# Optimization experiments

Measured on AMD Instinct MI355X. Metric: run time of the kernel, lower is better.

Reference implementation:

```python
import jax, jax.numpy as jnp
import numpy as np

N_HEAD = 16
D_MODEL = 2048
ROPE_BASE = 10000.0


def setup_inputs() -> dict:
    key = jax.random.key(0)
    k1, k2, k3 = jax.random.split(key, 3)
    b, s, d = 2, 2048, D_MODEL
    x = jax.random.normal(k1, (b, s, d), dtype=jnp.float32)
    # torch nn.Linear init scale ~ 1/sqrt(fan_in); keep activations sane
    W_qkv = jax.random.normal(k2, (3 * d, d), dtype=jnp.float32) * (d ** -0.5)
    W_o = jax.random.normal(k3, (d, d), dtype=jnp.float32) * (d ** -0.5)
    return {"x": x, "W_qkv": W_qkv, "W_o": W_o}


def _rotate_half(x):
    x1, x2 = jnp.split(x, 2, axis=-1)
    return jnp.concatenate((-x2, x1), axis=-1)


def _rope_cos_sin(seq_len, d_head, dtype):
    inv_freq = 1.0 / (ROPE_BASE ** (jnp.arange(0, d_head, 2, dtype=jnp.float32) / d_head))
    t = jnp.arange(seq_len, dtype=jnp.float32)
    freqs = jnp.einsum("i,j->ij", t, inv_freq)          # [s, d_head/2]
    emb = jnp.concatenate((freqs, freqs), axis=-1)       # [s, d_head]
    return jnp.cos(emb).astype(dtype)[None, None], jnp.sin(emb).astype(dtype)[None, None]


def reference(x, W_qkv, W_o):
    b, s, d = x.shape
    h = N_HEAD
    dh = d // h
    qkv = x @ W_qkv.T                                    # [b, s, 3d]
    qkv = qkv.reshape(b, s, 3, h, dh)
    q, k, v = (jnp.transpose(qkv[:, :, i], (0, 2, 1, 3)) for i in range(3))  # [b, h, s, dh]
    cos, sin = _rope_cos_sin(s, dh, x.dtype)
    q = q * cos + _rotate_half(q) * sin
    k = k * cos + _rotate_half(k) * sin
    scale = dh ** -0.5
    scores = jnp.einsum("bhqd,bhkd->bhqk", q, k) * scale  # [b, h, s, s]
    causal = jnp.tril(jnp.ones((s, s), dtype=bool))
    scores = jnp.where(causal[None, None], scores, jnp.finfo(scores.dtype).min)
    attn = jax.nn.softmax(scores, axis=-1)
    z = jnp.einsum("bhqk,bhkd->bhqd", attn, v)            # [b, h, s, dh]
    z = jnp.transpose(z, (0, 2, 1, 3)).reshape(b, s, d)
    return z @ W_o.T
```

## Files before the change

### kernel.cpp

```cpp
#include <hip/hip_runtime.h>
#include <stdint.h>
#include <stddef.h>

typedef __attribute__((ext_vector_type(8))) short bf16x8;
typedef __attribute__((ext_vector_type(4))) float f32x4;
typedef __attribute__((ext_vector_type(16))) float f32x16;
typedef __attribute__((ext_vector_type(4))) unsigned int u32x4;

#define AS1 __attribute__((address_space(1)))
#define AS3 __attribute__((address_space(3)))

__device__ __forceinline__ void gll16(const void* g, void* l) {
  __builtin_amdgcn_global_load_lds((const AS1 unsigned int*)g, (AS3 unsigned int*)l, 16, 0, 0);
}

__device__ __forceinline__ uint16_t f2bf(float f) {
  uint32_t u = __builtin_bit_cast(uint32_t, f);
  u += 0x7fffu + ((u >> 16) & 1u);
  return (uint16_t)(u >> 16);
}
__device__ __forceinline__ float bf2f(uint16_t h) {
  uint32_t u = ((uint32_t)h) << 16;
  return __builtin_bit_cast(float, u);
}
__device__ __forceinline__ uint32_t pack2bf(float lo, float hi) {
  return (uint32_t)f2bf(lo) | ((uint32_t)f2bf(hi) << 16);
}

#define BARRIER() do { asm volatile("" ::: "memory"); __builtin_amdgcn_s_barrier(); asm volatile("" ::: "memory"); } while (0)

__global__ void cvt_all(const float* __restrict__ x, const float* __restrict__ wqkv,
                        const float* __restrict__ wo,
                        uint16_t* __restrict__ xb, uint16_t* __restrict__ wqkvb,
                        uint16_t* __restrict__ wob) {
  int i = blockIdx.x * blockDim.x + threadIdx.x;
  const float* in; uint16_t* out; int off;
  if (i < 1048576)      { in = x;    out = xb;    off = i; }
  else if (i < 2621440) { in = wqkv; out = wqkvb; off = i - 1048576; }
  else                  { in = wo;   out = wob;   off = i - 2621440; }
  float4 a = reinterpret_cast<const float4*>(in)[2 * off];
  float4 b = reinterpret_cast<const float4*>(in)[2 * off + 1];
  union { uint16_t h[8]; u32x4 v; } u;
  u.h[0] = f2bf(a.x); u.h[1] = f2bf(a.y); u.h[2] = f2bf(a.z); u.h[3] = f2bf(a.w);
  u.h[4] = f2bf(b.x); u.h[5] = f2bf(b.y); u.h[6] = f2bf(b.z); u.h[7] = f2bf(b.w);
  reinterpret_cast<u32x4*>(out)[off] = u.v;
}

__global__ void rope_table(float* __restrict__ cosT, float* __restrict__ sinT) {
  int idx = blockIdx.x * blockDim.x + threadIdx.x;
  int s = idx >> 6, i = idx & 63;
  float invf = expf(-(float)i * (9.2103403719761836f / 64.0f));
  float f = (float)s * invf;
  cosT[idx] = cosf(f);
  sinT[idx] = sinf(f);
}

__global__ void rope_apply2(uint16_t* __restrict__ Qb, uint16_t* __restrict__ Kb,
                            const float* __restrict__ cosT, const float* __restrict__ sinT) {
  int idx = blockIdx.x * blockDim.x + threadIdx.x;
  uint16_t* buf = (idx < 4194304) ? Qb : Kb;
  int id = idx & 4194303;
  int i = id & 63;
  int s = (id >> 6) & 2047;
  int bh = id >> 17;
  size_t base = ((size_t)bh * 2048 + s) * 128;
  float x0 = bf2f(buf[base + i]);
  float x1 = bf2f(buf[base + i + 64]);
  float c = cosT[(s << 6) + i], sn = sinT[(s << 6) + i];
  buf[base + i]      = f2bf(x0 * c - x1 * sn);
  buf[base + i + 64] = f2bf(x1 * c + x0 * sn);
}

__global__ __launch_bounds__(512, 2) void gemm_qkv(
    const uint16_t* __restrict__ A,
    const uint16_t* __restrict__ B,
    uint16_t* __restrict__ Qb, uint16_t* __restrict__ Kb, uint16_t* __restrict__ Vt) {
  extern __shared__ uint16_t L[];
  const int t = threadIdx.x, lane = t & 63, w = t >> 6;
  const int fr = lane & 15, fg = lane >> 4;
  const int wm = w >> 2, wn = w & 3;
  const int flat = blockIdx.y * 16 + blockIdx.x;
  const int swz = (flat & 7) * 64 + (flat >> 3);
  const int m0 = (swz & 15) * 256, n0 = (swz >> 4) * 192;

  f32x4 acc[8][3];
#pragma unroll
  for (int i = 0; i < 8; i++)
#pragma unroll
    for (int j = 0; j < 3; j++) acc[i][j] = (f32x4)(0.0f);

#define STA(kt, half)                                                             \
  do {                                                                            \
    if ((kt) < 32) {                                                              \
      int g0_ = m0 + (half) * 128;                                                \
      uint16_t* dst_ = &L[((kt) & 1) * 28672 + (half) * 8192];                    \
      _Pragma("unroll")                                                           \
      for (int j_ = 0; j_ < 2; ++j_) {                                            \
        int c_ = t + j_ * 512;                                                    \
        int row_ = c_ >> 3, cc_ = c_ & 7, scc_ = cc_ ^ (row_ & 7);                \
        gll16(&A[(size_t)(g0_ + row_) * 2048 + (kt) * 64 + scc_ * 8],             \
              &dst_[(c_ & ~63) * 8]);                                             \
      }                                                                           \
    }                                                                             \
  } while (0)

#define STB(kt)                                                                   \
  do {                                                                            \
    if ((kt) < 32) {                                                              \
      uint16_t* dst_ = &L[((kt) & 1) * 28672 + 16384];                            \
      _Pragma("unroll")                                                           \
      for (int j_ = 0; j_ < 3; ++j_) {                                            \
        int c_ = t + j_ * 512;                                                    \
        int row_ = c_ >> 3, cc_ = c_ & 7, scc_ = cc_ ^ (row_ & 7);                \
        gll16(&B[(size_t)(n0 + row_) * 2048 + (kt) * 64 + scc_ * 8],              \
              &dst_[(c_ & ~63) * 8]);                                             \
      }                                                                           \
    }                                                                             \
  } while (0)

  auto LDA4 = [&](bf16x8 (&af)[8], int buf, int mh) {
#pragma unroll
    for (int mi = 0; mi < 4; ++mi)
#pragma unroll
      for (int ks = 0; ks < 2; ++ks) {
        int lr = (mh * 4 + mi) * 16 + fr;
        int ck = (ks * 4 + fg) ^ (lr & 7);
        af[mi * 2 + ks] = *(const bf16x8*)&L[buf * 28672 + wm * 8192 + lr * 64 + ck * 8];
      }
  };
  auto LDB = [&](bf16x8* bfr, int buf, int ni0, int nn) {
#pragma unroll
    for (int ni = 0; ni < 2; ++ni) {
      if (ni >= nn) break;
#pragma unroll
      for (int ks = 0; ks < 2; ++ks) {
        int rn = wn * 48 + (ni0 + ni) * 16 + fr;
        int ck = (ks * 4 + fg) ^ (rn & 7);
        bfr[ni * 2 + ks] = *(const bf16x8*)&L[buf * 28672 + 16384 + rn * 64 + ck * 8];
      }
    }
  };
  auto MF = [&](bf16x8 (&af)[8], bf16x8* bfr, int mh, int ni0, int nn) {
    __builtin_amdgcn_s_setprio(1);
#pragma unroll
    for (int mi = 0; mi < 4; ++mi)
#pragma unroll
      for (int ni = 0; ni < 2; ++ni) {
        if (ni >= nn) break;
#pragma unroll
        for (int ks = 0; ks < 2; ++ks)
          acc[mh * 4 + mi][ni0 + ni] = __builtin_amdgcn_mfma_f32_16x16x32_bf16(
              af[mi * 2 + ks], bfr[ni * 2 + ks], acc[mh * 4 + mi][ni0 + ni], 0, 0, 0);
      }
    __builtin_amdgcn_s_setprio(0);
  };

  STA(0, 0); STA(0, 1); STB(0); STA(1, 0);
  asm volatile("s_waitcnt vmcnt(2)" ::: "memory");
  BARRIER();

  for (int tl = 0; tl < 32; ++tl) {
    const int buf = tl & 1;
    bf16x8 af[8], bA[4], bB[4];
    LDA4(af, buf, 0); LDB(bA, buf, 0, 2); STA(tl + 1, 1);
    BARRIER(); MF(af, bA, 0, 0, 2); BARRIER();
    LDB(bB, buf, 2, 1); STB(tl + 1);
    BARRIER(); MF(af, bB, 0, 2, 1); BARRIER();
    LDA4(af, buf, 1);
    BARRIER(); MF(af, bA, 1, 0, 2); BARRIER();
    STA(tl + 2, 0);
    BARRIER(); MF(af, bB, 1, 2, 1);
    if (tl < 30) asm volatile("s_waitcnt vmcnt(2)" ::: "memory");
    else         asm volatile("s_waitcnt vmcnt(0)" ::: "memory");
    BARRIER();
  }
#undef STA
#undef STB

#pragma unroll
  for (int mi = 0; mi < 8; ++mi) {
#pragma unroll
    for (int ni = 0; ni < 3; ++ni) {
      int ng = n0 + wn * 48 + ni * 16 + fr;
      int head = (ng >> 7) & 15, dd = ng & 127;
      if (ng < 4096) {
        uint16_t* dst = (ng < 2048) ? Qb : Kb;
#pragma unroll
        for (int r = 0; r < 4; r++) {
          int mg = m0 + wm * 128 + mi * 16 + fg * 4 + r;
          int b = mg >> 11, si = mg & 2047;
          dst[((size_t)(b * 16 + head) * 2048 + si) * 128 + dd] = f2bf(acc[mi][ni][r]);
        }
      } else {
        uint2 pv = make_uint2(pack2bf(acc[mi][ni][0], acc[mi][ni][1]),
                              pack2bf(acc[mi][ni][2], acc[mi][ni][3]));
        int mg = m0 + wm * 128 + mi * 16 + fg * 4;
        int b = mg >> 11, si = mg & 2047;
        *(uint2*)&Vt[((size_t)(b * 16 + head) * 128 + dd) * 2048 + si] = pv;
      }
    }
  }
}

__global__ __launch_bounds__(256) void gemm_out_k(
    const uint16_t* __restrict__ A,
    const uint16_t* __restrict__ B,
    float* __restrict__ C) {
  __shared__ uint16_t Ash[3][128 * 32];
  __shared__ uint16_t Bsh[3][128 * 32];
  const int t = threadIdx.x;
  const int lane = t & 63;
  const int w = t >> 6, wr = w >> 1, wc = w & 1;
  const int fr = lane & 15, fg = lane >> 4, fk = fg * 8;
  const int m0 = blockIdx.x * 128, n0 = blockIdx.y * 128;
  const int K = 2048;
  const int T = K / 32;
  const int c0 = t, c1 = t + 256;

  f32x4 acc[4][4];
#pragma unroll
  for (int i = 0; i < 4; i++)
#pragma unroll
    for (int j = 0; j < 4; j++) acc[i][j] = (f32x4)(0.0f);

#define OUT_STAGE(tile, buf)                                                        \
  {                                                                                 \
    int kt_ = (tile) * 32;                                                          \
    gll16(&A[(size_t)(m0 + (c0 >> 2)) * K + kt_ + (c0 & 3) * 8], &Ash[buf][(c0 & ~63) * 8]); \
    gll16(&A[(size_t)(m0 + (c1 >> 2)) * K + kt_ + (c1 & 3) * 8], &Ash[buf][(c1 & ~63) * 8]); \
    gll16(&B[(size_t)(n0 + (c0 >> 2)) * K + kt_ + (c0 & 3) * 8], &Bsh[buf][(c0 & ~63) * 8]); \
    gll16(&B[(size_t)(n0 + (c1 >> 2)) * K + kt_ + (c1 & 3) * 8], &Bsh[buf][(c1 & ~63) * 8]); \
  }

  OUT_STAGE(0, 0);
  OUT_STAGE(1, 1);
  asm volatile("s_waitcnt vmcnt(4)" ::: "memory");
  BARRIER();

  for (int tl = 0; tl < T; ++tl) {
    const int cur = tl % 3;
    if (tl + 2 < T) OUT_STAGE(tl + 2, (tl + 2) % 3);
    bf16x8 af[4], bfr[4];
#pragma unroll
    for (int mi = 0; mi < 4; mi++) af[mi] = *(const bf16x8*)&Ash[cur][(wr * 64 + mi * 16 + fr) * 32 + fk];
#pragma unroll
    for (int ni = 0; ni < 4; ni++) bfr[ni] = *(const bf16x8*)&Bsh[cur][(wc * 64 + ni * 16 + fr) * 32 + fk];
    __builtin_amdgcn_s_setprio(1);
#pragma unroll
    for (int mi = 0; mi < 4; mi++)
#pragma unroll
      for (int ni = 0; ni < 4; ni++)
        acc[mi][ni] = __builtin_amdgcn_mfma_f32_16x16x32_bf16(af[mi], bfr[ni], acc[mi][ni], 0, 0, 0);
    __builtin_amdgcn_s_setprio(0);
    if (tl + 2 < T) {
      asm volatile("s_waitcnt vmcnt(4)" ::: "memory");
    } else {
      asm volatile("s_waitcnt vmcnt(0)" ::: "memory");
    }
    BARRIER();
  }
#undef OUT_STAGE

#pragma unroll
  for (int mi = 0; mi < 4; mi++) {
#pragma unroll
    for (int ni = 0; ni < 4; ni++) {
      int ng = n0 + wc * 64 + ni * 16 + fr;
#pragma unroll
      for (int r = 0; r < 4; r++) {
        int mg = m0 + wr * 64 + mi * 16 + fg * 4 + r;
        C[(size_t)mg * 2048 + ng] = acc[mi][ni][r];
      }
    }
  }
}

__device__ __forceinline__ bf16x8 mk_pa(uint32_t p0, uint32_t p1, uint32_t p2, uint32_t p3, int hi) {
  uint32_t x0 = (uint32_t)__shfl_xor((int)p0, 32, 64);
  uint32_t x1 = (uint32_t)__shfl_xor((int)p1, 32, 64);
  uint32_t x2 = (uint32_t)__shfl_xor((int)p2, 32, 64);
  uint32_t x3 = (uint32_t)__shfl_xor((int)p3, 32, 64);
  u32x4 v;
  v[0] = hi ? x2 : p0;
  v[1] = hi ? x3 : p1;
  v[2] = hi ? p2 : x0;
  v[3] = hi ? p3 : x1;
  return __builtin_bit_cast(bf16x8, v);
}

__global__ __launch_bounds__(256, 2) void attn_kernel(
    const uint16_t* __restrict__ Qb, const uint16_t* __restrict__ Kb,
    const uint16_t* __restrict__ Vt, uint16_t* __restrict__ zb) {
  __shared__ uint16_t Ksh[2][64 * 128];
  __shared__ uint16_t Vsh[2][128 * 64];

  const int t = threadIdx.x, lane = t & 63, w = t >> 6;
  const int l31 = lane & 31, hi = lane >> 5;
  const int bx = blockIdx.x, bh = blockIdx.y;
  const int qt = (bh & 16) ? (15 - bx) : bx;
  const int q0 = qt * 128;
  const int qg = q0 + w * 32 + l31;
  const size_t hbase = (size_t)bh * 2048 * 128;
  const float scale2 = 0.08838834764831845f * 1.4426950408889634f;

#define ATT_STAGE(kt, buf)                                                        \
  do {                                                                            \
    const uint16_t* Kg_ = Kb + hbase + (size_t)(kt) * 64 * 128;                   \
    const uint16_t* Vg_ = Vt + hbase + (size_t)(kt) * 64;                         \
    _Pragma("unroll")                                                             \
    for (int i_ = 0; i_ < 4; i_++) {                                              \
      int c_ = t + i_ * 256;                                                      \
      { int row_ = c_ >> 4, cc_ = c_ & 15, scc_ = cc_ ^ (row_ & 7);               \
        gll16(&Kg_[row_ * 128 + scc_ * 8], &Ksh[buf][(c_ & ~63) * 8]); }          \
      { int r_ = c_ >> 3, cc_ = c_ & 7, scc_ = cc_ ^ (r_ & 7);                    \
        gll16(&Vg_[(size_t)r_ * 2048 + scc_ * 8], &Vsh[buf][(c_ & ~63) * 8]); }   \
    }                                                                             \
  } while (0)

  bf16x8 qf[8];
#pragma unroll
  for (int dc = 0; dc < 8; ++dc)
    qf[dc] = *(const bf16x8*)&Qb[hbase + (size_t)qg * 128 + dc * 16 + hi * 8];

  f32x16 oacc[4];
#pragma unroll
  for (int i = 0; i < 4; i++) oacc[i] = (f32x16)(0.0f);
  float mrow = -1e30f, lrow = 0.0f;

  const int ktiles = 2 * qt + 2;
  ATT_STAGE(0, 0);
  asm volatile("s_waitcnt vmcnt(0)" ::: "memory");
  BARRIER();

  for (int kt = 0; kt < ktiles; ++kt) {
    const int cur = kt & 1;
    if (kt + 1 < ktiles) ATT_STAGE(kt + 1, cur ^ 1);

    const int kv_base = kt * 64;
    if (kv_base <= q0 + w * 32 + 31) {
      f32x16 s0 = (f32x16)(0.0f), s1 = (f32x16)(0.0f);
      __builtin_amdgcn_s_setprio(1);
#pragma unroll
      for (int dc = 0; dc < 8; ++dc) {
        int ch = dc * 2 + hi;
        bf16x8 k0 = *(const bf16x8*)&Ksh[cur][l31 * 128 + ((ch ^ (l31 & 7)) * 8)];
        bf16x8 k1 = *(const bf16x8*)&Ksh[cur][(32 + l31) * 128 + ((ch ^ (l31 & 7)) * 8)];
        s0 = __builtin_amdgcn_mfma_f32_32x32x16_bf16(k0, qf[dc], s0, 0, 0, 0);
        s1 = __builtin_amdgcn_mfma_f32_32x32x16_bf16(k1, qf[dc], s1, 0, 0, 0);
      }
      __builtin_amdgcn_s_setprio(0);

      const bool need_mask = (kv_base + 63 > q0 + w * 32);
#pragma unroll
      for (int reg = 0; reg < 16; ++reg) {
        int koff = (reg & 3) + 8 * (reg >> 2) + 4 * hi;
        float a0 = s0[reg] * scale2, a1 = s1[reg] * scale2;
        if (need_mask) {
          if (kv_base + koff > qg) a0 = -1e30f;
          if (kv_base + 32 + koff > qg) a1 = -1e30f;
        }
        s0[reg] = a0; s1[reg] = a1;
      }

      float pmax = -1e30f;
#pragma unroll
      for (int reg = 0; reg < 16; ++reg) pmax = fmaxf(pmax, fmaxf(s0[reg], s1[reg]));
      pmax = fmaxf(pmax, __shfl_xor(pmax, 32, 64));

      bool defer = __all(pmax <= mrow + 8.0f);
      if (!defer) {
        float mnew = fmaxf(mrow, pmax);
        float al = exp2f(mrow - mnew);
        lrow *= al;
#pragma unroll
        for (int reg = 0; reg < 16; ++reg) {
          int src = (reg & 3) + 8 * (reg >> 2) + 4 * hi;
          float ar = __shfl(al, src, 64);
#pragma unroll
          for (int n = 0; n < 4; ++n) oacc[n][reg] *= ar;
        }
        mrow = mnew;
      }

      float ps = 0.0f;
      uint32_t pk0[8], pk1[8];
#pragma unroll
      for (int i = 0; i < 8; ++i) {
        float a = exp2f(s0[2 * i] - mrow), b = exp2f(s0[2 * i + 1] - mrow);
        ps += a + b;
        pk0[i] = pack2bf(a, b);
        float c = exp2f(s1[2 * i] - mrow), d = exp2f(s1[2 * i + 1] - mrow);
        ps += c + d;
        pk1[i] = pack2bf(c, d);
      }
      ps += __shfl_xor(ps, 32, 64);
      lrow += ps;

      bf16x8 pa[4];
      pa[0] = mk_pa(pk0[0], pk0[1], pk0[2], pk0[3], hi);
      pa[1] = mk_pa(pk0[4], pk0[5], pk0[6], pk0[7], hi);
      pa[2] = mk_pa(pk1[0], pk1[1], pk1[2], pk1[3], hi);
      pa[3] = mk_pa(pk1[4], pk1[5], pk1[6], pk1[7], hi);

      __builtin_amdgcn_s_setprio(1);
#pragma unroll
      for (int ksl = 0; ksl < 4; ++ksl) {
        int ch = ksl * 2 + hi;
#pragma unroll
        for (int n = 0; n < 4; ++n) {
          int d = n * 32 + l31;
          bf16x8 vf = *(const bf16x8*)&Vsh[cur][d * 64 + ((ch ^ (d & 7)) * 8)];
          oacc[n] = __builtin_amdgcn_mfma_f32_32x32x16_bf16(pa[ksl], vf, oacc[n], 0, 0, 0);
        }
      }
      __builtin_amdgcn_s_setprio(0);
    }

    asm volatile("s_waitcnt vmcnt(0)" ::: "memory");
    BARRIER();
  }
#undef ATT_STAGE

  const int b = bh >> 4, h = bh & 15;
#pragma unroll
  for (int reg = 0; reg < 16; ++reg) {
    int rloc = (reg & 3) + 8 * (reg >> 2) + 4 * hi;
    float linv = 1.0f / __shfl(lrow, rloc, 64);
    int rowg = q0 + w * 32 + rloc;
    size_t base = ((size_t)b * 2048 + rowg) * 2048 + h * 128 + l31;
#pragma unroll
    for (int n = 0; n < 4; ++n)
      zb[base + n * 32] = f2bf(oacc[n][reg] * linv);
  }
}

extern "C" void kernel_launch(void* const* d_in, const int* in_sizes, int n_in,
                              void* d_out, int out_size, void* d_ws, size_t ws_size,
                              hipStream_t stream) {
  const float* x    = (const float*)d_in[0];
  const float* Wqkv = (const float*)d_in[1];
  const float* Wo   = (const float*)d_in[2];
  float* out = (float*)d_out;
  char* ws = (char*)d_ws;

  uint16_t* Qb    = (uint16_t*)(ws + 0);
  uint16_t* Kb    = (uint16_t*)(ws + 16777216);
  uint16_t* Vt    = (uint16_t*)(ws + 33554432);
  uint16_t* xb    = (uint16_t*)(ws + 50331648);
  uint16_t* zb    = (uint16_t*)(ws + 50331648);
  uint16_t* wqkvb = (uint16_t*)(ws + 67108864);
  uint16_t* wob   = (uint16_t*)(ws + 92274688);
  float*    cosT  = (float*)   (ws + 100663296);
  float*    sinT  = (float*)   (ws + 101187584);

  cvt_all<<<12288, 256, 0, stream>>>(x, Wqkv, Wo, xb, wqkvb, wob);
  rope_table<<<512, 256, 0, stream>>>(cosT, sinT);

  gemm_qkv<<<dim3(16, 32), 512, 114688, stream>>>(xb, wqkvb, Qb, Kb, Vt);

  rope_apply2<<<32768, 256, 0, stream>>>(Qb, Kb, cosT, sinT);

  attn_kernel<<<dim3(16, 32), 256, 0, stream>>>(Qb, Kb, Vt, zb);

  gemm_out_k<<<dim3(32, 16), 256, 0, stream>>>(zb, wob, out);
}
```

Measured before the change: 294.0 us.

## Restructure output GEMM tiling and use hardware bf16 pack conversion

The output projection GEMM moves from 128x128 tiles with 256 threads and a 3-stage 32-wide K pipeline to 256x128 tiles with 512 threads. It now uses a double-buffered 64-wide K pipeline with XOR-swizzled LDS, loads interleaved with MFMA phases, and a grouped block-order swizzle for L2 reuse. Separately, the software bf16 rounding-and-pack is replaced by the v_cvt_pk_bf16_f32 instruction in the QKV GEMM V store and the attention P packing. The attention softmax also uses tree reductions for the row max and sum to shorten dependency chains. The extra barriers in the GEMM and the different rounding path could offset some of the gains.

```diff
diff --git a/kernel.cpp b/kernel.cpp
--- a/kernel.cpp
+++ b/kernel.cpp
@@ -23,8 +23,10 @@
   uint32_t u = ((uint32_t)h) << 16;
   return __builtin_bit_cast(float, u);
 }
-__device__ __forceinline__ uint32_t pack2bf(float lo, float hi) {
-  return (uint32_t)f2bf(lo) | ((uint32_t)f2bf(hi) << 16);
+__device__ __forceinline__ uint32_t cvtpk(float lo, float hi) {
+  uint32_t r;
+  asm("v_cvt_pk_bf16_f32 %0, %1, %2" : "=v"(r) : "v"(lo), "v"(hi));
+  return r;
 }
 
 #define BARRIER() do { asm volatile("" ::: "memory"); __builtin_amdgcn_s_barrier(); asm volatile("" ::: "memory"); } while (0)
@@ -192,8 +194,8 @@
           dst[((size_t)(b * 16 + head) * 2048 + si) * 128 + dd] = f2bf(acc[mi][ni][r]);
         }
       } else {
-        uint2 pv = make_uint2(pack2bf(acc[mi][ni][0], acc[mi][ni][1]),
-                              pack2bf(acc[mi][ni][2], acc[mi][ni][3]));
+        uint2 pv = make_uint2(cvtpk(acc[mi][ni][0], acc[mi][ni][1]),
+                              cvtpk(acc[mi][ni][2], acc[mi][ni][3]));
         int mg = m0 + wm * 128 + mi * 16 + fg * 4;
         int b = mg >> 11, si = mg & 2047;
         *(uint2*)&Vt[((size_t)(b * 16 + head) * 128 + dd) * 2048 + si] = pv;
@@ -202,73 +204,112 @@
   }
 }
 
-__global__ __launch_bounds__(256) void gemm_out_k(
+__global__ __launch_bounds__(512, 2) void gemm_out_k(
     const uint16_t* __restrict__ A,
     const uint16_t* __restrict__ B,
     float* __restrict__ C) {
-  __shared__ uint16_t Ash[3][128 * 32];
-  __shared__ uint16_t Bsh[3][128 * 32];
-  const int t = threadIdx.x;
-  const int lane = t & 63;
-  const int w = t >> 6, wr = w >> 1, wc = w & 1;
-  const int fr = lane & 15, fg = lane >> 4, fk = fg * 8;
-  const int m0 = blockIdx.x * 128, n0 = blockIdx.y * 128;
-  const int K = 2048;
-  const int T = K / 32;
-  const int c0 = t, c1 = t + 256;
-
-  f32x4 acc[4][4];
-#pragma unroll
-  for (int i = 0; i < 4; i++)
-#pragma unroll
-    for (int j = 0; j < 4; j++) acc[i][j] = (f32x4)(0.0f);
-
-#define OUT_STAGE(tile, buf)                                                        \
-  {                                                                                 \
-    int kt_ = (tile) * 32;                                                          \
-    gll16(&A[(size_t)(m0 + (c0 >> 2)) * K + kt_ + (c0 & 3) * 8], &Ash[buf][(c0 & ~63) * 8]); \
-    gll16(&A[(size_t)(m0 + (c1 >> 2)) * K + kt_ + (c1 & 3) * 8], &Ash[buf][(c1 & ~63) * 8]); \
-    gll16(&B[(size_t)(n0 + (c0 >> 2)) * K + kt_ + (c0 & 3) * 8], &Bsh[buf][(c0 & ~63) * 8]); \
-    gll16(&B[(size_t)(n0 + (c1 >> 2)) * K + kt_ + (c1 & 3) * 8], &Bsh[buf][(c1 & ~63) * 8]); \
-  }
-
-  OUT_STAGE(0, 0);
-  OUT_STAGE(1, 1);
-  asm volatile("s_waitcnt vmcnt(4)" ::: "memory");
+  extern __shared__ uint16_t L[];
+  const int t = threadIdx.x, lane = t & 63, w = t >> 6;
+  const int fr = lane & 15, fg = lane >> 4;
+  const int wm = w >> 2, wn = w & 3;
+  const int flat = blockIdx.y * 16 + blockIdx.x;
+  const int swz = (flat & 7) * 32 + (flat >> 3);
+  const int m0 = (swz & 15) * 256, n0 = (swz >> 4) * 128;
+
+  f32x4 acc[8][2];
+#pragma unroll
+  for (int i = 0; i < 8; i++)
+#pragma unroll
+    for (int j = 0; j < 2; j++) acc[i][j] = (f32x4)(0.0f);
+
+#define STA(kt, half)                                                             \
+  do {                                                                            \
+    if ((kt) < 32) {                                                              \
+      int g0_ = m0 + (half) * 128;                                                \
+      uint16_t* dst_ = &L[((kt) & 1) * 24576 + (half) * 8192];                    \
+      _Pragma("unroll")                                                           \
+      for (int j_ = 0; j_ < 2; ++j_) {                                            \
+        int c_ = t + j_ * 512;                                                    \
+        int row_ = c_ >> 3, cc_ = c_ & 7, scc_ = cc_ ^ (row_ & 7);                \
+        gll16(&A[(size_t)(g0_ + row_) * 2048 + (kt) * 64 + scc_ * 8],             \
+              &dst_[(c_ & ~63) * 8]);                                             \
+      }                                                                           \
+    }                                                                             \
+  } while (0)
+
+#define STB(kt)                                                                   \
+  do {                                                                            \
+    if ((kt) < 32) {                                                              \
+      uint16_t* dst_ = &L[((kt) & 1) * 24576 + 16384];                            \
+      _Pragma("unroll")                                                           \
+      for (int j_ = 0; j_ < 2; ++j_) {                                            \
+        int c_ = t + j_ * 512;                                                    \
+        int row_ = c_ >> 3, cc_ = c_ & 7, scc_ = cc_ ^ (row_ & 7);                \
+        gll16(&B[(size_t)(n0 + row_) * 2048 + (kt) * 64 + scc_ * 8],              \
+              &dst_[(c_ & ~63) * 8]);                                             \
+      }                                                                           \
+    }                                                                             \
+  } while (0)
+
+  auto LDA4 = [&](bf16x8 (&af)[8], int buf, int mh) {
+#pragma unroll
+    for (int mi = 0; mi < 4; ++mi)
+#pragma unroll
+      for (int ks = 0; ks < 2; ++ks) {
+        int lr = (mh * 4 + mi) * 16 + fr;
+        int ck = (ks * 4 + fg) ^ (lr & 7);
+        af[mi * 2 + ks] = *(const bf16x8*)&L[buf * 24576 + wm * 8192 + lr * 64 + ck * 8];
+      }
+  };
+  auto LDB1 = [&](bf16x8 (&bfr)[2], int buf, int ni) {
+#pragma unroll
+    for (int ks = 0; ks < 2; ++ks) {
+      int rn = wn * 32 + ni * 16 + fr;
+      int ck = (ks * 4 + fg) ^ (rn & 7);
+      bfr[ks] = *(const bf16x8*)&L[buf * 24576 + 16384 + rn * 64 + ck * 8];
+    }
+  };
+  auto MF1 = [&](bf16x8 (&af)[8], bf16x8 (&bfr)[2], int mh, int ni) {
+    __builtin_amdgcn_s_setprio(1);
+#pragma unroll
+    for (int mi = 0; mi < 4; ++mi)
+#pragma unroll
+      for (int ks = 0; ks < 2; ++ks)
+        acc[mh * 4 + mi][ni] = __builtin_amdgcn_mfma_f32_16x16x32_bf16(
+            af[mi * 2 + ks], bfr[ks], acc[mh * 4 + mi][ni], 0, 0, 0);
+    __builtin_amdgcn_s_setprio(0);
+  };
+
+  STA(0, 0); STA(0, 1); STB(0); STA(1, 0);
+  asm volatile("s_waitcnt vmcnt(2)" ::: "memory");
   BARRIER();
 
-  for (int tl = 0; tl < T; ++tl) {
-    const int cur = tl % 3;
-    if (tl + 2 < T) OUT_STAGE(tl + 2, (tl + 2) % 3);
-    bf16x8 af[4], bfr[4];
-#pragma unroll
-    for (int mi = 0; mi < 4; mi++) af[mi] = *(const bf16x8*)&Ash[cur][(wr * 64 + mi * 16 + fr) * 32 + fk];
-#pragma unroll
-    for (int ni = 0; ni < 4; ni++) bfr[ni] = *(const bf16x8*)&Bsh[cur][(wc * 64 + ni * 16 + fr) * 32 + fk];
-    __builtin_amdgcn_s_setprio(1);
-#pragma unroll
-    for (int mi = 0; mi < 4; mi++)
-#pragma unroll
-      for (int ni = 0; ni < 4; ni++)
-        acc[mi][ni] = __builtin_amdgcn_mfma_f32_16x16x32_bf16(af[mi], bfr[ni], acc[mi][ni], 0, 0, 0);
-    __builtin_amdgcn_s_setprio(0);
-    if (tl + 2 < T) {
-      asm volatile("s_waitcnt vmcnt(4)" ::: "memory");
-    } else {
-      asm volatile("s_waitcnt vmcnt(0)" ::: "memory");
-    }
+  for (int tl = 0; tl < 32; ++tl) {
+    const int buf = tl & 1;
+    bf16x8 af[8], bA[2], bB[2];
+    LDA4(af, buf, 0); LDB1(bA, buf, 0); STA(tl + 1, 1);
+    BARRIER(); MF1(af, bA, 0, 0); BARRIER();
+    LDB1(bB, buf, 1); STB(tl + 1);
+    BARRIER(); MF1(af, bB, 0, 1); BARRIER();
+    LDA4(af, buf, 1);
+    BARRIER(); MF1(af, bA, 1, 0); BARRIER();
+    STA(tl + 2, 0);
+    BARRIER(); MF1(af, bB, 1, 1);
+    if (tl < 30) asm volatile("s_waitcnt vmcnt(2)" ::: "memory");
+    else         asm volatile("s_waitcnt vmcnt(0)" ::: "memory");
     BARRIER();
   }
-#undef OUT_STAGE
-
-#pragma unroll
-  for (int mi = 0; mi < 4; mi++) {
-#pragma unroll
-    for (int ni = 0; ni < 4; ni++) {
-      int ng = n0 + wc * 64 + ni * 16 + fr;
+#undef STA
+#undef STB
+
+#pragma unroll
+  for (int mi = 0; mi < 8; ++mi) {
+#pragma unroll
+    for (int ni = 0; ni < 2; ++ni) {
+      int ng = n0 + wn * 32 + ni * 16 + fr;
 #pragma unroll
       for (int r = 0; r < 4; r++) {
-        int mg = m0 + wr * 64 + mi * 16 + fg * 4 + r;
+        int mg = m0 + wm * 128 + mi * 16 + fg * 4 + r;
         C[(size_t)mg * 2048 + ng] = acc[mi][ni][r];
       }
     }
@@ -362,9 +403,12 @@
         s0[reg] = a0; s1[reg] = a1;
       }
 
-      float pmax = -1e30f;
-#pragma unroll
-      for (int reg = 0; reg < 16; ++reg) pmax = fmaxf(pmax, fmaxf(s0[reg], s1[reg]));
+      float m8[8];
+#pragma unroll
+      for (int i = 0; i < 8; ++i)
+        m8[i] = fmaxf(fmaxf(s0[i], s0[i + 8]), fmaxf(s1[i], s1[i + 8]));
+      float pmax = fmaxf(fmaxf(fmaxf(m8[0], m8[4]), fmaxf(m8[1], m8[5])),
+                         fmaxf(fmaxf(m8[2], m8[6]), fmaxf(m8[3], m8[7])));
       pmax = fmaxf(pmax, __shfl_xor(pmax, 32, 64));
 
       bool defer = __all(pmax <= mrow + 8.0f);
@@ -382,17 +426,18 @@
         mrow = mnew;
       }
 
-      float ps = 0.0f;
+      float ps0 = 0.0f, ps1 = 0.0f, ps2 = 0.0f, ps3 = 0.0f;
       uint32_t pk0[8], pk1[8];
 #pragma unroll
       for (int i = 0; i < 8; ++i) {
         float a = exp2f(s0[2 * i] - mrow), b = exp2f(s0[2 * i + 1] - mrow);
-        ps += a + b;
-        pk0[i] = pack2bf(a, b);
+        ps0 += a; ps1 += b;
+        pk0[i] = cvtpk(a, b);
         float c = exp2f(s1[2 * i] - mrow), d = exp2f(s1[2 * i + 1] - mrow);
-        ps += c + d;
-        pk1[i] = pack2bf(c, d);
-      }
+        ps2 += c; ps3 += d;
+        pk1[i] = cvtpk(c, d);
+      }
+      float ps = (ps0 + ps1) + (ps2 + ps3);
       ps += __shfl_xor(ps, 32, 64);
       lrow += ps;
 
@@ -462,5 +507,5 @@
 
   attn_kernel<<<dim3(16, 32), 256, 0, stream>>>(Qb, Kb, Vt, zb);
 
-  gemm_out_k<<<dim3(32, 16), 256, 0, stream>>>(zb, wob, out);
-}
+  gemm_out_k<<<dim3(16, 16), 512, 98304, stream>>>(zb, wob, out);
+}
```

Result: faster. 277.4 us (-5.6%).
